# Optimization experiments

Hardware: AMD Instinct MI355X
Metric: run time of the kernel (lower is better)

Reference implementation:

```python
import jax, jax.numpy as jnp
import numpy as np

B, S, D_IN, D_OUT, RANK = 4, 2048, 4096, 4096, 16
ALPHA = 16
SCALING = ALPHA / RANK  # 1.0


def setup_inputs() -> dict:
    key = jax.random.key(0)
    k_x, k_q, k_b, k_a, k_bb = jax.random.split(key, 5)
    x = jax.random.normal(k_x, (B, S, D_IN), dtype=jnp.float32)
    # int4 symmetric quantized weight values in [-8, 7], stored as int32
    qweight = jax.random.randint(k_q, (D_OUT, D_IN), -8, 8, dtype=jnp.int32)
    # per-tensor scale (abs_max / 7 in the original); a plausible small value
    scales = jnp.array([0.01], dtype=jnp.float32)
    bias = jax.random.normal(k_b, (D_OUT,), dtype=jnp.float32) * 0.02
    # LoRA params (acting as "trained" values; original inits A kaiming, B zeros)
    lora_A = jax.random.normal(k_a, (D_IN, RANK), dtype=jnp.float32) * (1.0 / np.sqrt(D_IN))
    lora_B = jax.random.normal(k_bb, (RANK, D_OUT), dtype=jnp.float32) * 0.01
    return {"x": x, "qweight": qweight, "scales": scales, "bias": bias,
            "lora_A": lora_A, "lora_B": lora_B}


def reference(x, qweight, scales, bias, lora_A, lora_B):
    # dequantize: int4 values * scalar scale -> fp32 weight [D_OUT, D_IN]
    w = qweight.astype(jnp.float32) * scales[0]
    # F.linear(x, w, bias): x @ w.T + bias
    out = jnp.einsum('bsd,od->bso', x, w) + bias
    # LoRA low-rank path: (x @ A) @ B * scaling (dropout=0 -> identity)
    lora_out = (x @ lora_A) @ lora_B
    return out + lora_out * SCALING
```

## Files before the change

### kernel.cpp

```cpp
#include <hip/hip_runtime.h>
#include <stdint.h>
#include <math.h>


static constexpr int Mdim = 8192;
static constexpr int Ndim = 4096;
static constexpr int Kdim = 4096;

typedef __bf16 bf16x8 __attribute__((ext_vector_type(8)));
typedef float f32x4 __attribute__((ext_vector_type(4)));
typedef int   i32x4 __attribute__((ext_vector_type(4)));

__device__ __forceinline__ void async_copy16(const void* gptr, void* lptr) {
    auto g = (const __attribute__((address_space(1))) unsigned char*)(uintptr_t)gptr;
    auto l = (__attribute__((address_space(3))) unsigned char*)(uintptr_t)lptr;
    __builtin_amdgcn_global_load_lds(g, l, 16, 0, 0);
}

static constexpr int BLK_W = Ndim * Kdim / (256 * 16);
static constexpr int BLK_X = Mdim;
static constexpr int BLK_BT = Ndim / 256;

__global__ void __launch_bounds__(256) prep_kernel(
        const float* __restrict__ x,
        const int* __restrict__ qw,
        const float* __restrict__ lA,
        const float* __restrict__ lB,
        int8_t* __restrict__ x_i8,
        int8_t* __restrict__ w_i8,
        int8_t* __restrict__ a_i8t,
        __bf16* __restrict__ Blbt,
        float* __restrict__ row_scale,
        float* __restrict__ a_scale_g) {
    __shared__ float red[8];
    int b = blockIdx.x;
    const int tid = threadIdx.x;

    if (b == 0) {
        float am = 0.f;
        const float4* ap = (const float4*)lA + tid * 64;
        for (int i = 0; i < 64; ++i) {
            float4 v = ap[i];
            am = fmaxf(am, fmaxf(fmaxf(fabsf(v.x), fabsf(v.y)),
                                 fmaxf(fabsf(v.z), fabsf(v.w))));
        }
        for (int off = 32; off; off >>= 1) am = fmaxf(am, __shfl_xor(am, off));
        if ((tid & 63) == 0) red[tid >> 6] = am;
        __syncthreads();
        if (tid == 0) {
            float m = fmaxf(fmaxf(red[0], red[1]), fmaxf(red[2], red[3]));
            red[4] = m;
            a_scale_g[0] = m > 0.f ? m / 127.f : 0.f;
        }
        __syncthreads();
        float amax = red[4];
        float inv = amax > 0.f ? 127.f / amax : 0.f;
        int k0 = tid * 16;
#pragma unroll
        for (int r = 0; r < 16; ++r) {
            int8_t o[16];
#pragma unroll
            for (int kk = 0; kk < 16; ++kk) {
                float v = lA[(size_t)(k0 + kk) * 16 + r];
                o[kk] = (int8_t)(int)rintf(v * inv);
            }
            *(i32x4*)(a_i8t + (size_t)r * Kdim + k0) = *(i32x4*)o;
        }
        return;
    }
    b -= 1;

    if (b < BLK_W) {
        size_t idx = ((size_t)b * 256 + tid) * 16;
        const int4* q = (const int4*)(qw + idx);
        int4 q0 = q[0], q1 = q[1], q2 = q[2], q3 = q[3];
        int8_t o[16] = {(int8_t)q0.x, (int8_t)q0.y, (int8_t)q0.z, (int8_t)q0.w,
                        (int8_t)q1.x, (int8_t)q1.y, (int8_t)q1.z, (int8_t)q1.w,
                        (int8_t)q2.x, (int8_t)q2.y, (int8_t)q2.z, (int8_t)q2.w,
                        (int8_t)q3.x, (int8_t)q3.y, (int8_t)q3.z, (int8_t)q3.w};
        *(i32x4*)(w_i8 + idx) = *(i32x4*)o;
        return;
    }
    b -= BLK_W;

    if (b < BLK_X) {
        const int row = b;
        const float4* xp = (const float4*)(x + (size_t)row * Kdim) + tid * 4;
        float4 v0 = xp[0], v1 = xp[1], v2 = xp[2], v3 = xp[3];
        float am = 0.f;
        am = fmaxf(am, fmaxf(fmaxf(fabsf(v0.x), fabsf(v0.y)), fmaxf(fabsf(v0.z), fabsf(v0.w))));
        am = fmaxf(am, fmaxf(fmaxf(fabsf(v1.x), fabsf(v1.y)), fmaxf(fabsf(v1.z), fabsf(v1.w))));
        am = fmaxf(am, fmaxf(fmaxf(fabsf(v2.x), fabsf(v2.y)), fmaxf(fabsf(v2.z), fabsf(v2.w))));
        am = fmaxf(am, fmaxf(fmaxf(fabsf(v3.x), fabsf(v3.y)), fmaxf(fabsf(v3.z), fabsf(v3.w))));
        for (int off = 32; off; off >>= 1) am = fmaxf(am, __shfl_xor(am, off));
        if ((tid & 63) == 0) red[tid >> 6] = am;
        __syncthreads();
        if (tid == 0) {
            float m = fmaxf(fmaxf(red[0], red[1]), fmaxf(red[2], red[3]));
            red[4] = m;
            row_scale[row] = m > 0.f ? m / 127.f : 0.f;
        }
        __syncthreads();
        float amax = red[4];
        float inv = amax > 0.f ? 127.f / amax : 0.f;
        float vv[16] = {v0.x, v0.y, v0.z, v0.w, v1.x, v1.y, v1.z, v1.w,
                        v2.x, v2.y, v2.z, v2.w, v3.x, v3.y, v3.z, v3.w};
        int8_t o[16];
#pragma unroll
        for (int i = 0; i < 16; ++i) o[i] = (int8_t)(int)rintf(vv[i] * inv);
        *(i32x4*)(x_i8 + (size_t)row * Kdim + tid * 16) = *(i32x4*)o;
        return;
    }
    b -= BLK_X;

    {
        int c = b * 256 + tid;
        __bf16 tmp[16];
#pragma unroll
        for (int r = 0; r < 16; ++r) tmp[r] = (__bf16)lB[(size_t)r * Ndim + c];
        *(bf16x8*)(Blbt + (size_t)c * 16) = *(bf16x8*)tmp;
        *(bf16x8*)(Blbt + (size_t)c * 16 + 8) = *(bf16x8*)(tmp + 8);
    }
}

__global__ void __launch_bounds__(256) xa_kernel(
        const int8_t* __restrict__ x_i8,
        const int8_t* __restrict__ a_i8t,
        const float* __restrict__ row_scale,
        const float* __restrict__ a_scale_g,
        __bf16* __restrict__ xab) {
    __shared__ __align__(16) char sX[64 * 64];
    __shared__ __align__(16) char sAq[16 * 64];
    const int tid = threadIdx.x, wave = tid >> 6, lane = tid & 63;
    const int quad = lane >> 4, l16 = lane & 15;
    const int bm = blockIdx.x;
    const size_t xbase = ((size_t)bm * 64 + (tid >> 2)) * Kdim + (tid & 3) * 16;
    i32x4 acc = {0, 0, 0, 0};
    for (int k0 = 0; k0 < Kdim; k0 += 64) {
        __syncthreads();
        async_copy16(x_i8 + xbase + k0, sX + tid * 16);
        if (tid < 64)
            async_copy16(a_i8t + (size_t)(tid >> 2) * Kdim + (tid & 3) * 16 + k0,
                         sAq + tid * 16);
        __syncthreads();
        i32x4 af = *(const i32x4*)(sX + (wave * 16 + l16) * 64 + quad * 16);
        i32x4 bf = *(const i32x4*)(sAq + l16 * 64 + quad * 16);
        acc = __builtin_amdgcn_mfma_i32_16x16x64_i8(af, bf, acc, 0, 0, 0);
    }
    const float asc = a_scale_g[0];
    const int rl = wave * 16 + quad * 4;
#pragma unroll
    for (int r = 0; r < 4; ++r) {
        int grow = bm * 64 + rl + r;
        float v = (float)acc[r] * row_scale[grow] * asc;
        xab[(size_t)grow * 16 + l16] = (__bf16)v;
    }
}

__global__ void __launch_bounds__(256) gemm_kernel(
        const int8_t* __restrict__ Xq,
        const int8_t* __restrict__ Wq,
        const float* __restrict__ scales,
        const float* __restrict__ bias,
        const float* __restrict__ row_scale,
        const __bf16* __restrict__ xab,
        const __bf16* __restrict__ Blbt,
        float* __restrict__ out) {
    __shared__ __align__(16) char smem[16384 + 512];
    char* sA = smem;
    char* sB = smem + 8192;

    const int tid = threadIdx.x, wave = tid >> 6, lane = tid & 63;
    const int wm = wave >> 1, wn = wave & 1;
    const int quad = lane >> 4, l16 = lane & 15;
    const int bm = blockIdx.y, bn = blockIdx.x;

    const int arow = tid >> 2;
    const int acolb = (tid & 3) * 16;
    const size_t a_base = (size_t)(bm * 128 + arow) * Kdim + acolb;
    const size_t b_base = (size_t)(bn * 128 + arow) * Kdim + acolb;

    i32x4 acc[4][4];
#pragma unroll
    for (int i = 0; i < 4; ++i)
#pragma unroll
        for (int j = 0; j < 4; ++j) acc[i][j] = i32x4{0, 0, 0, 0};

    for (int k0 = 0; k0 < Kdim; k0 += 64) {
        __syncthreads();
        async_copy16(Xq + a_base + k0,                     sA + tid * 16);
        async_copy16(Xq + a_base + (size_t)64 * Kdim + k0, sA + 4096 + tid * 16);
        async_copy16(Wq + b_base + k0,                     sB + tid * 16);
        async_copy16(Wq + b_base + (size_t)64 * Kdim + k0, sB + 4096 + tid * 16);
        __syncthreads();

        i32x4 aF[4], bF[4];
#pragma unroll
        for (int i = 0; i < 4; ++i)
            aF[i] = *(const i32x4*)(sA + (wm * 64 + i * 16 + l16) * 64 + quad * 16);
#pragma unroll
        for (int j = 0; j < 4; ++j)
            bF[j] = *(const i32x4*)(sB + (wn * 64 + j * 16 + l16) * 64 + quad * 16);

#pragma unroll
        for (int i = 0; i < 4; ++i)
#pragma unroll
            for (int j = 0; j < 4; ++j)
                acc[i][j] = __builtin_amdgcn_mfma_i32_16x16x64_i8(aF[i], bF[j], acc[i][j], 0, 0, 0);
    }

    const float wsc = scales[0];
    float bj4[4];
#pragma unroll
    for (int j = 0; j < 4; ++j) bj4[j] = bias[bn * 128 + wn * 64 + j * 16 + l16];

    __syncthreads();
    async_copy16((const char*)(xab + (size_t)bm * 128 * 16) + tid * 16, smem + tid * 16);
    async_copy16((const char*)(Blbt + (size_t)bn * 128 * 16) + tid * 16, smem + 4096 + tid * 16);
    if (tid < 32)
        async_copy16((const char*)(row_scale + bm * 128) + tid * 16, smem + 8192 + tid * 16);
    __syncthreads();

    const __bf16* sXA = (const __bf16*)smem;
    const __bf16* sBL = (const __bf16*)(smem + 4096);
    const float*  sRS = (const float*)(smem + 8192);

    bf16x8 zf;
#pragma unroll
    for (int k = 0; k < 8; ++k) zf[k] = (__bf16)0.f;

    bf16x8 aF2[4], bF2[4];
#pragma unroll
    for (int i = 0; i < 4; ++i) {
        if (quad < 2) aF2[i] = *(const bf16x8*)(sXA + (wm * 64 + i * 16 + l16) * 16 + quad * 8);
        else          aF2[i] = zf;
    }
#pragma unroll
    for (int j = 0; j < 4; ++j) {
        if (quad < 2) bF2[j] = *(const bf16x8*)(sBL + (wn * 64 + j * 16 + l16) * 16 + quad * 8);
        else          bF2[j] = zf;
    }

    f32x4 lacc[4][4];
#pragma unroll
    for (int j = 0; j < 4; ++j)
#pragma unroll
        for (int i = 0; i < 4; ++i)
            lacc[i][j] = f32x4{bj4[j], bj4[j], bj4[j], bj4[j]};

#pragma unroll
    for (int i = 0; i < 4; ++i)
#pragma unroll
        for (int j = 0; j < 4; ++j)
            lacc[i][j] = __builtin_amdgcn_mfma_f32_16x16x32_bf16(aF2[i], bF2[j], lacc[i][j], 0, 0, 0);

    const int col0 = bn * 128 + wn * 64 + l16;
    const int rl0 = wm * 64 + quad * 4;
#pragma unroll
    for (int j = 0; j < 4; ++j) {
        const int col = col0 + j * 16;
#pragma unroll
        for (int i = 0; i < 4; ++i) {
            const int lr = rl0 + i * 16;
#pragma unroll
            for (int r = 0; r < 4; ++r) {
                float sx = sRS[lr + r] * wsc;
                out[(size_t)(bm * 128 + lr + r) * Ndim + col] =
                    (float)acc[i][j][r] * sx + lacc[i][j][r];
            }
        }
    }
}

extern "C" void kernel_launch(void* const* d_in, const int* in_sizes, int n_in,
                              void* d_out, int out_size, void* d_ws, size_t ws_size,
                              hipStream_t stream) {
    const float* x      = (const float*)d_in[0];
    const int*   qw     = (const int*)d_in[1];
    const float* scales = (const float*)d_in[2];
    const float* bias   = (const float*)d_in[3];
    const float* lA     = (const float*)d_in[4];
    const float* lB     = (const float*)d_in[5];
    float* out = (float*)d_out;

    char* ws = (char*)d_ws;
    int8_t* x_i8   = (int8_t*)ws;
    int8_t* w_i8   = (int8_t*)(ws + 33554432);
    int8_t* a_i8t  = (int8_t*)(ws + 50331648);
    __bf16* xab    = (__bf16*)(ws + 50397184);
    __bf16* Blbt   = (__bf16*)(ws + 50659328);
    float* row_scale = (float*)(ws + 50790400);
    float* a_scale_g = (float*)(ws + 50823168);

    const int prep_blocks = 1 + BLK_W + BLK_X + BLK_BT;
    prep_kernel<<<prep_blocks, 256, 0, stream>>>(
        x, qw, lA, lB, x_i8, w_i8, a_i8t, Blbt, row_scale, a_scale_g);
    xa_kernel<<<Mdim / 64, 256, 0, stream>>>(x_i8, a_i8t, row_scale, a_scale_g, xab);
    dim3 grid(Ndim / 128, Mdim / 128);
    gemm_kernel<<<grid, 256, 0, stream>>>(x_i8, w_i8, scales, bias, row_scale,
                                          xab, Blbt, out);
}
```

Before: 474.3 us.

## Pre-swizzle int8 operands into MFMA fragment order and drop LDS staging in GEMM

The prep kernel now writes quantized X, W and LoRA A in a slab layout that matches the MFMA 16x16x64 fragment order, one 1 KiB slab per wave per k-step. The GEMM and xa kernels then load fragments straight from global memory with coalesced 16-byte per-lane reads, with no LDS staging and no __syncthreads inside the K loop. This removes the barrier and LDS traffic cost. In exchange, operands shared by the waves of a block are no longer reused through LDS, so each wave fetches its own A/B slabs from L2/global, and there is no explicit prefetch to hide latency. Prep also changes work decomposition, with 16 rows per block and a per-row amax computed via 16-lane shuffles.

```diff
diff --git a/kernel.cpp b/kernel.cpp
--- a/kernel.cpp
+++ b/kernel.cpp
@@ -17,8 +17,8 @@
     __builtin_amdgcn_global_load_lds(g, l, 16, 0, 0);
 }
 
-static constexpr int BLK_W = Ndim * Kdim / (256 * 16);
-static constexpr int BLK_X = Mdim;
+static constexpr int BLK_X = Mdim / 16;
+static constexpr int BLK_W = Ndim / 16;
 static constexpr int BLK_BT = Ndim / 256;
 
 __global__ void __launch_bounds__(256) prep_kernel(
@@ -26,9 +26,9 @@
         const int* __restrict__ qw,
         const float* __restrict__ lA,
         const float* __restrict__ lB,
-        int8_t* __restrict__ x_i8,
-        int8_t* __restrict__ w_i8,
-        int8_t* __restrict__ a_i8t,
+        int8_t* __restrict__ Xs,
+        int8_t* __restrict__ Bs,
+        int8_t* __restrict__ a_i8,
         __bf16* __restrict__ Blbt,
         float* __restrict__ row_scale,
         float* __restrict__ a_scale_g) {
@@ -36,149 +36,149 @@
     int b = blockIdx.x;
     const int tid = threadIdx.x;
 
+    if (b < BLK_X) {
+        const int m0 = b * 16;
+        const int r = tid >> 4, u = tid & 15;
+        const float4* xrow4 = (const float4*)(x + (size_t)(m0 + r) * Kdim + u * 256);
+        float am = 0.f;
+        for (int q = 0; q < 64; ++q) {
+            float4 v = xrow4[q];
+            am = fmaxf(am, fmaxf(fmaxf(fabsf(v.x), fabsf(v.y)),
+                                 fmaxf(fabsf(v.z), fabsf(v.w))));
+        }
+#pragma unroll
+        for (int off = 1; off < 16; off <<= 1) am = fmaxf(am, __shfl_xor(am, off, 16));
+        if (u == 0) row_scale[m0 + r] = am > 0.f ? am / 127.f : 0.f;
+        const float inv = am > 0.f ? 127.f / am : 0.f;
+        const int bm = b >> 3, wm = (b >> 2) & 1, islab = b & 3;
+#pragma unroll 4
+        for (int j = 0; j < 16; ++j) {
+            const int c = u * 16 + j;
+            const int k0 = c >> 2, quad = c & 3;
+            int8_t o[16];
+#pragma unroll
+            for (int p = 0; p < 4; ++p) {
+                float4 v = xrow4[j * 4 + p];
+                o[p * 4 + 0] = (int8_t)(int)rintf(v.x * inv);
+                o[p * 4 + 1] = (int8_t)(int)rintf(v.y * inv);
+                o[p * 4 + 2] = (int8_t)(int)rintf(v.z * inv);
+                o[p * 4 + 3] = (int8_t)(int)rintf(v.w * inv);
+            }
+            const size_t slab = (size_t)(((bm * 64 + k0) * 2 + wm) * 4 + islab);
+            *(i32x4*)(Xs + slab * 1024 + (quad * 16 + r) * 16) = *(i32x4*)o;
+        }
+        return;
+    }
+    b -= BLK_X;
+
+    if (b < BLK_W) {
+        const int n0 = b * 16;
+        const int r = tid >> 4, u = tid & 15;
+        const int* qrow = qw + (size_t)(n0 + r) * Kdim + u * 256;
+        const int bn = b >> 3, wn = (b >> 2) & 1, jslab = b & 3;
+#pragma unroll 4
+        for (int j = 0; j < 16; ++j) {
+            const int c = u * 16 + j;
+            const int k0 = c >> 2, quad = c & 3;
+            const int4* q4 = (const int4*)(qrow + j * 16);
+            int4 q0 = q4[0], q1 = q4[1], q2 = q4[2], q3 = q4[3];
+            int8_t o[16] = {(int8_t)q0.x, (int8_t)q0.y, (int8_t)q0.z, (int8_t)q0.w,
+                            (int8_t)q1.x, (int8_t)q1.y, (int8_t)q1.z, (int8_t)q1.w,
+                            (int8_t)q2.x, (int8_t)q2.y, (int8_t)q2.z, (int8_t)q2.w,
+                            (int8_t)q3.x, (int8_t)q3.y, (int8_t)q3.z, (int8_t)q3.w};
+            const size_t slab = (size_t)(((bn * 64 + k0) * 2 + wn) * 4 + jslab);
+            *(i32x4*)(Bs + slab * 1024 + (quad * 16 + r) * 16) = *(i32x4*)o;
+        }
+        return;
+    }
+    b -= BLK_W;
+
     if (b == 0) {
         float am = 0.f;
         const float4* ap = (const float4*)lA + tid * 64;
-        for (int i = 0; i < 64; ++i) {
-            float4 v = ap[i];
+        for (int q = 0; q < 64; ++q) {
+            float4 v = ap[q];
             am = fmaxf(am, fmaxf(fmaxf(fabsf(v.x), fabsf(v.y)),
                                  fmaxf(fabsf(v.z), fabsf(v.w))));
         }
-        for (int off = 32; off; off >>= 1) am = fmaxf(am, __shfl_xor(am, off));
+#pragma unroll
+        for (int off = 1; off < 64; off <<= 1) am = fmaxf(am, __shfl_xor(am, off));
         if ((tid & 63) == 0) red[tid >> 6] = am;
         __syncthreads();
-        if (tid == 0) {
-            float m = fmaxf(fmaxf(red[0], red[1]), fmaxf(red[2], red[3]));
-            red[4] = m;
-            a_scale_g[0] = m > 0.f ? m / 127.f : 0.f;
-        }
-        __syncthreads();
-        float amax = red[4];
-        float inv = amax > 0.f ? 127.f / amax : 0.f;
-        int k0 = tid * 16;
-#pragma unroll
-        for (int r = 0; r < 16; ++r) {
+        const float amax = fmaxf(fmaxf(red[0], red[1]), fmaxf(red[2], red[3]));
+        if (tid == 0) a_scale_g[0] = amax > 0.f ? amax / 127.f : 0.f;
+        const float inv = amax > 0.f ? 127.f / amax : 0.f;
+        const int rho = tid & 15, u = tid >> 4;
+        for (int j = 0; j < 16; ++j) {
+            const int c = u * 16 + j;
+            const int k0 = c >> 2, quad = c & 3;
             int8_t o[16];
 #pragma unroll
-            for (int kk = 0; kk < 16; ++kk) {
-                float v = lA[(size_t)(k0 + kk) * 16 + r];
-                o[kk] = (int8_t)(int)rintf(v * inv);
-            }
-            *(i32x4*)(a_i8t + (size_t)r * Kdim + k0) = *(i32x4*)o;
+            for (int kk = 0; kk < 16; ++kk)
+                o[kk] = (int8_t)(int)rintf(lA[(size_t)(c * 16 + kk) * 16 + rho] * inv);
+            *(i32x4*)(a_i8 + (size_t)k0 * 1024 + (quad * 16 + rho) * 16) = *(i32x4*)o;
         }
         return;
     }
     b -= 1;
 
-    if (b < BLK_W) {
-        size_t idx = ((size_t)b * 256 + tid) * 16;
-        const int4* q = (const int4*)(qw + idx);
-        int4 q0 = q[0], q1 = q[1], q2 = q[2], q3 = q[3];
-        int8_t o[16] = {(int8_t)q0.x, (int8_t)q0.y, (int8_t)q0.z, (int8_t)q0.w,
-                        (int8_t)q1.x, (int8_t)q1.y, (int8_t)q1.z, (int8_t)q1.w,
-                        (int8_t)q2.x, (int8_t)q2.y, (int8_t)q2.z, (int8_t)q2.w,
-                        (int8_t)q3.x, (int8_t)q3.y, (int8_t)q3.z, (int8_t)q3.w};
-        *(i32x4*)(w_i8 + idx) = *(i32x4*)o;
-        return;
-    }
-    b -= BLK_W;
-
-    if (b < BLK_X) {
-        const int row = b;
-        const float4* xp = (const float4*)(x + (size_t)row * Kdim) + tid * 4;
-        float4 v0 = xp[0], v1 = xp[1], v2 = xp[2], v3 = xp[3];
-        float am = 0.f;
-        am = fmaxf(am, fmaxf(fmaxf(fabsf(v0.x), fabsf(v0.y)), fmaxf(fabsf(v0.z), fabsf(v0.w))));
-        am = fmaxf(am, fmaxf(fmaxf(fabsf(v1.x), fabsf(v1.y)), fmaxf(fabsf(v1.z), fabsf(v1.w))));
-        am = fmaxf(am, fmaxf(fmaxf(fabsf(v2.x), fabsf(v2.y)), fmaxf(fabsf(v2.z), fabsf(v2.w))));
-        am = fmaxf(am, fmaxf(fmaxf(fabsf(v3.x), fabsf(v3.y)), fmaxf(fabsf(v3.z), fabsf(v3.w))));
-        for (int off = 32; off; off >>= 1) am = fmaxf(am, __shfl_xor(am, off));
-        if ((tid & 63) == 0) red[tid >> 6] = am;
-        __syncthreads();
-        if (tid == 0) {
-            float m = fmaxf(fmaxf(red[0], red[1]), fmaxf(red[2], red[3]));
-            red[4] = m;
-            row_scale[row] = m > 0.f ? m / 127.f : 0.f;
-        }
-        __syncthreads();
-        float amax = red[4];
-        float inv = amax > 0.f ? 127.f / amax : 0.f;
-        float vv[16] = {v0.x, v0.y, v0.z, v0.w, v1.x, v1.y, v1.z, v1.w,
-                        v2.x, v2.y, v2.z, v2.w, v3.x, v3.y, v3.z, v3.w};
-        int8_t o[16];
-#pragma unroll
-        for (int i = 0; i < 16; ++i) o[i] = (int8_t)(int)rintf(vv[i] * inv);
-        *(i32x4*)(x_i8 + (size_t)row * Kdim + tid * 16) = *(i32x4*)o;
-        return;
-    }
-    b -= BLK_X;
-
     {
-        int c = b * 256 + tid;
+        const int c = b * 256 + tid;
         __bf16 tmp[16];
 #pragma unroll
-        for (int r = 0; r < 16; ++r) tmp[r] = (__bf16)lB[(size_t)r * Ndim + c];
+        for (int rr = 0; rr < 16; ++rr) tmp[rr] = (__bf16)lB[(size_t)rr * Ndim + c];
         *(bf16x8*)(Blbt + (size_t)c * 16) = *(bf16x8*)tmp;
         *(bf16x8*)(Blbt + (size_t)c * 16 + 8) = *(bf16x8*)(tmp + 8);
     }
 }
 
 __global__ void __launch_bounds__(256) xa_kernel(
-        const int8_t* __restrict__ x_i8,
-        const int8_t* __restrict__ a_i8t,
+        const int8_t* __restrict__ Xs,
+        const int8_t* __restrict__ a_i8,
         const float* __restrict__ row_scale,
         const float* __restrict__ a_scale_g,
         __bf16* __restrict__ xab) {
-    __shared__ __align__(16) char sX[64 * 64];
-    __shared__ __align__(16) char sAq[16 * 64];
     const int tid = threadIdx.x, wave = tid >> 6, lane = tid & 63;
     const int quad = lane >> 4, l16 = lane & 15;
-    const int bm = blockIdx.x;
-    const size_t xbase = ((size_t)bm * 64 + (tid >> 2)) * Kdim + (tid & 3) * 16;
+    const int bm2 = blockIdx.x;
+    const int bm = bm2 >> 1, wm = bm2 & 1;
+    const int8_t* aptr = Xs + (size_t)((bm * 64 * 2 + wm) * 4 + wave) * 1024 + lane * 16;
+    const int8_t* bptr = a_i8 + lane * 16;
     i32x4 acc = {0, 0, 0, 0};
-    for (int k0 = 0; k0 < Kdim; k0 += 64) {
-        __syncthreads();
-        async_copy16(x_i8 + xbase + k0, sX + tid * 16);
-        if (tid < 64)
-            async_copy16(a_i8t + (size_t)(tid >> 2) * Kdim + (tid & 3) * 16 + k0,
-                         sAq + tid * 16);
-        __syncthreads();
-        i32x4 af = *(const i32x4*)(sX + (wave * 16 + l16) * 64 + quad * 16);
-        i32x4 bf = *(const i32x4*)(sAq + l16 * 64 + quad * 16);
+#pragma unroll 4
+    for (int k0 = 0; k0 < 64; ++k0) {
+        i32x4 af = *(const i32x4*)(aptr + (size_t)k0 * 8192);
+        i32x4 bf = *(const i32x4*)(bptr + (size_t)k0 * 1024);
         acc = __builtin_amdgcn_mfma_i32_16x16x64_i8(af, bf, acc, 0, 0, 0);
     }
     const float asc = a_scale_g[0];
     const int rl = wave * 16 + quad * 4;
 #pragma unroll
     for (int r = 0; r < 4; ++r) {
-        int grow = bm * 64 + rl + r;
+        const int grow = bm2 * 64 + rl + r;
         float v = (float)acc[r] * row_scale[grow] * asc;
         xab[(size_t)grow * 16 + l16] = (__bf16)v;
     }
 }
 
-__global__ void __launch_bounds__(256) gemm_kernel(
-        const int8_t* __restrict__ Xq,
-        const int8_t* __restrict__ Wq,
+__global__ void __launch_bounds__(256) gemm_flat(
+        const int8_t* __restrict__ Xs,
+        const int8_t* __restrict__ Bs,
         const float* __restrict__ scales,
         const float* __restrict__ bias,
         const float* __restrict__ row_scale,
         const __bf16* __restrict__ xab,
         const __bf16* __restrict__ Blbt,
         float* __restrict__ out) {
-    __shared__ __align__(16) char smem[16384 + 512];
-    char* sA = smem;
-    char* sB = smem + 8192;
+    __shared__ __align__(16) char smem[8704];
 
     const int tid = threadIdx.x, wave = tid >> 6, lane = tid & 63;
     const int wm = wave >> 1, wn = wave & 1;
     const int quad = lane >> 4, l16 = lane & 15;
     const int bm = blockIdx.y, bn = blockIdx.x;
 
-    const int arow = tid >> 2;
-    const int acolb = (tid & 3) * 16;
-    const size_t a_base = (size_t)(bm * 128 + arow) * Kdim + acolb;
-    const size_t b_base = (size_t)(bn * 128 + arow) * Kdim + acolb;
+    const int8_t* aptr = Xs + (size_t)((bm * 64 * 2 + wm) * 4) * 1024 + lane * 16;
+    const int8_t* bptr = Bs + (size_t)((bn * 64 * 2 + wn) * 4) * 1024 + lane * 16;
 
     i32x4 acc[4][4];
 #pragma unroll
@@ -186,22 +186,15 @@
 #pragma unroll
         for (int j = 0; j < 4; ++j) acc[i][j] = i32x4{0, 0, 0, 0};
 
-    for (int k0 = 0; k0 < Kdim; k0 += 64) {
-        __syncthreads();
-        async_copy16(Xq + a_base + k0,                     sA + tid * 16);
-        async_copy16(Xq + a_base + (size_t)64 * Kdim + k0, sA + 4096 + tid * 16);
-        async_copy16(Wq + b_base + k0,                     sB + tid * 16);
-        async_copy16(Wq + b_base + (size_t)64 * Kdim + k0, sB + 4096 + tid * 16);
-        __syncthreads();
-
+#pragma unroll 2
+    for (int k0 = 0; k0 < 64; ++k0) {
         i32x4 aF[4], bF[4];
 #pragma unroll
         for (int i = 0; i < 4; ++i)
-            aF[i] = *(const i32x4*)(sA + (wm * 64 + i * 16 + l16) * 64 + quad * 16);
+            aF[i] = *(const i32x4*)(aptr + (size_t)k0 * 8192 + i * 1024);
 #pragma unroll
         for (int j = 0; j < 4; ++j)
-            bF[j] = *(const i32x4*)(sB + (wn * 64 + j * 16 + l16) * 64 + quad * 16);
-
+            bF[j] = *(const i32x4*)(bptr + (size_t)k0 * 8192 + j * 1024);
 #pragma unroll
         for (int i = 0; i < 4; ++i)
 #pragma unroll
@@ -214,7 +207,6 @@
 #pragma unroll
     for (int j = 0; j < 4; ++j) bj4[j] = bias[bn * 128 + wn * 64 + j * 16 + l16];
 
-    __syncthreads();
     async_copy16((const char*)(xab + (size_t)bm * 128 * 16) + tid * 16, smem + tid * 16);
     async_copy16((const char*)(Blbt + (size_t)bn * 128 * 16) + tid * 16, smem + 4096 + tid * 16);
     if (tid < 32)
@@ -264,7 +256,7 @@
             const int lr = rl0 + i * 16;
 #pragma unroll
             for (int r = 0; r < 4; ++r) {
-                float sx = sRS[lr + r] * wsc;
+                const float sx = sRS[lr + r] * wsc;
                 out[(size_t)(bm * 128 + lr + r) * Ndim + col] =
                     (float)acc[i][j][r] * sx + lacc[i][j][r];
             }
@@ -284,19 +276,19 @@
     float* out = (float*)d_out;
 
     char* ws = (char*)d_ws;
-    int8_t* x_i8   = (int8_t*)ws;
-    int8_t* w_i8   = (int8_t*)(ws + 33554432);
-    int8_t* a_i8t  = (int8_t*)(ws + 50331648);
+    int8_t* Xs     = (int8_t*)ws;
+    int8_t* Bs     = (int8_t*)(ws + 33554432);
+    int8_t* a_i8   = (int8_t*)(ws + 50331648);
     __bf16* xab    = (__bf16*)(ws + 50397184);
     __bf16* Blbt   = (__bf16*)(ws + 50659328);
     float* row_scale = (float*)(ws + 50790400);
     float* a_scale_g = (float*)(ws + 50823168);
 
-    const int prep_blocks = 1 + BLK_W + BLK_X + BLK_BT;
+    const int prep_blocks = BLK_X + BLK_W + 1 + BLK_BT;
     prep_kernel<<<prep_blocks, 256, 0, stream>>>(
-        x, qw, lA, lB, x_i8, w_i8, a_i8t, Blbt, row_scale, a_scale_g);
-    xa_kernel<<<Mdim / 64, 256, 0, stream>>>(x_i8, a_i8t, row_scale, a_scale_g, xab);
+        x, qw, lA, lB, Xs, Bs, a_i8, Blbt, row_scale, a_scale_g);
+    xa_kernel<<<Mdim / 64, 256, 0, stream>>>(Xs, a_i8, row_scale, a_scale_g, xab);
     dim3 grid(Ndim / 128, Mdim / 128);
-    gemm_kernel<<<grid, 256, 0, stream>>>(x_i8, w_i8, scales, bias, row_scale,
-                                          xab, Blbt, out);
-}
+    gemm_flat<<<grid, 256, 0, stream>>>(Xs, Bs, scales, bias, row_scale,
+                                        xab, Blbt, out);
+}
```

Result: slower. 519.8 us (+9.6%).
